# Kernel optimization log

Measured on AMD Instinct MI355X. Metric: run time of the kernel, lower is better.

## Reference

```python
import jax, jax.numpy as jnp
import numpy as np

B, T, I, E, K, J = 4, 4096, 1024, 16, 512, 1024

def setup_inputs() -> dict:
    key = jax.random.key(0)
    k1, k2, k3 = jax.random.split(key, 3)
    X = jax.random.normal(k1, (B, T, I), dtype=jnp.float32)
    ind = jax.random.randint(k2, (B, E, K), 0, T, dtype=jnp.int64)
    W = jax.random.normal(k3, (E, I, J), dtype=jnp.float32)
    return {"X": X, "ind": ind, "W": W}

def reference(X, ind, W):
    b, t, i = X.shape
    # offset each batch's indices into the flattened [B*T, I] token table
    offset = jnp.arange(b, dtype=ind.dtype)[:, None, None] * t  # [B,1,1]
    X_flat = X.reshape(b * t, i)
    X_gathered = X_flat[ind + offset]  # [B,E,K,I] irregular gather
    Y = jnp.einsum('beki,eij->bekj', X_gathered, W)  # grouped GEMM per expert
    return Y
```

## Files before the change

kernel.cpp:

```cpp
#include <hip/hip_runtime.h>

#define DI __device__ __forceinline__

constexpr int Bc = 4, Tc = 4096, Ic = 1024, Ec = 16, Kc = 512, Jc = 1024;

typedef __attribute__((ext_vector_type(8))) short short8;
typedef __attribute__((ext_vector_type(4))) float floatx4;

DI unsigned pack2_bf16(float a, float b) {
  union { float f; unsigned u; } ua, ub;
  ua.f = a; ub.f = b;
  const unsigned x = ua.u + 0x8000u;
  const unsigned y = ub.u + 0x8000u;
#if __has_builtin(__builtin_amdgcn_perm)
  return __builtin_amdgcn_perm(y, x, 0x07060302u);
#else
  return (x >> 16) | (y & 0xFFFF0000u);
#endif
}

DI void async_load16(const void* g, void* lds) {
  __builtin_amdgcn_global_load_lds((const __attribute__((address_space(1))) void*)g,
                                   (__attribute__((address_space(3))) void*)lds,
                                   16, 0, 0);
}

__global__ __launch_bounds__(256) void transpose_w(const float* __restrict__ W,
                                                   unsigned short* __restrict__ Wt) {
  __shared__ float tile[64][65];
  const int bid = blockIdx.x;
  const int jt = bid & 15;
  const int it = (bid >> 4) & 15;
  const int e  = bid >> 8;
  const int t  = threadIdx.x;

  const float* Wp = W + ((size_t)e * Ic + (size_t)it * 64) * Jc + jt * 64;
  const int jl  = (t & 15) * 4;
  const int il0 = t >> 4;
#pragma unroll
  for (int p = 0; p < 4; ++p) {
    const int il = p * 16 + il0;
    const float4 v = *(const float4*)(Wp + (size_t)il * Jc + jl);
    tile[il][jl + 0] = v.x; tile[il][jl + 1] = v.y;
    tile[il][jl + 2] = v.z; tile[il][jl + 3] = v.w;
  }
  __syncthreads();
  unsigned short* Wo = Wt + ((size_t)e * Jc + (size_t)jt * 64) * Ic + it * 64;
  const int ilw = (t & 15) * 4;
  const int jl0 = t >> 4;
#pragma unroll
  for (int p = 0; p < 4; ++p) {
    const int jlw = p * 16 + jl0;
    uint2 u;
    u.x = pack2_bf16(tile[ilw + 0][jlw], tile[ilw + 1][jlw]);
    u.y = pack2_bf16(tile[ilw + 2][jlw], tile[ilw + 3][jlw]);
    *(uint2*)(Wo + (size_t)jlw * Ic + ilw) = u;
  }
}

__global__ __launch_bounds__(256) void moe_gemm(const float* __restrict__ X,
                                                const int* __restrict__ ind,
                                                const unsigned short* __restrict__ Wt,
                                                float* __restrict__ Y) {
  __shared__ unsigned short As[128 * 32];
  __shared__ unsigned short Bs[128 * 32];
  __shared__ unsigned long long rowA[128];

  const int bid = blockIdx.x;
  const int jt = bid & 7;
  const int kt = (bid >> 3) & 3;
  const int e  = (bid >> 5) & 15;
  const int b  = bid >> 9;

  const int t = threadIdx.x;
  const int w = t >> 6;
  const int l = t & 63;

  if (t < 128) {
    const int r = ind[((b * Ec + e) * Kc) + kt * 128 + t];
    rowA[t] = (unsigned long long)(const void*)X +
              ((unsigned long long)(b * Tc + r) * (unsigned long long)Ic) * 4ull;
  }
  __syncthreads();

  const int c4 = (t & 7) * 4;
  unsigned long long abase[4];
#pragma unroll
  for (int p = 0; p < 4; ++p)
    abase[p] = rowA[p * 32 + (t >> 3)] + (unsigned long long)(c4 * 4);
  unsigned short* awr = &As[(t >> 3) * 32 + c4];

  const unsigned short* bsrc0 =
      Wt + ((size_t)(e * Jc + jt * 128 + (w * 2 + 0) * 16 + (l >> 2))) * Ic + (l & 3) * 8;
  const unsigned short* bsrc1 =
      Wt + ((size_t)(e * Jc + jt * 128 + (w * 2 + 1) * 16 + (l >> 2))) * Ic + (l & 3) * 8;
  unsigned short* bdst0 = &Bs[(w * 2 + 0) * 16 * 32];
  unsigned short* bdst1 = &Bs[(w * 2 + 1) * 16 * 32];

  floatx4 acc[4][4];
#pragma unroll
  for (int tm = 0; tm < 4; ++tm)
#pragma unroll
    for (int tn = 0; tn < 4; ++tn) acc[tm][tn] = (floatx4){0.f, 0.f, 0.f, 0.f};

  const int wm = (w & 1) * 64;
  const int wn = (w >> 1) * 64;
  const int lrow = l & 15;
  const int quad = l >> 4;

  for (int kk = 0; kk < Ic / 32; ++kk) {
    float4 av[4];
#pragma unroll
    for (int p = 0; p < 4; ++p)
      av[p] = *reinterpret_cast<const float4*>(abase[p] + (unsigned long long)(kk * 128));

    __syncthreads();

    async_load16(bsrc0 + kk * 32, bdst0);
    async_load16(bsrc1 + kk * 32, bdst1);

#pragma unroll
    for (int p = 0; p < 4; ++p) {
      uint2 u;
      u.x = pack2_bf16(av[p].x, av[p].y);
      u.y = pack2_bf16(av[p].z, av[p].w);
      *(uint2*)(awr + p * 1024) = u;
    }
    __syncthreads();

    short8 af[4], bf[4];
#pragma unroll
    for (int tm = 0; tm < 4; ++tm)
      af[tm] = *(const short8*)&As[(wm + tm * 16 + lrow) * 32 + quad * 8];
#pragma unroll
    for (int tn = 0; tn < 4; ++tn)
      bf[tn] = *(const short8*)&Bs[(wn + tn * 16 + lrow) * 32 + quad * 8];
#pragma unroll
    for (int tm = 0; tm < 4; ++tm)
#pragma unroll
      for (int tn = 0; tn < 4; ++tn)
        acc[tm][tn] = __builtin_amdgcn_mfma_f32_16x16x32_bf16(af[tm], bf[tn], acc[tm][tn], 0, 0, 0);
  }

  float* Yp = Y + ((size_t)(b * Ec + e) * Kc + (size_t)kt * 128) * Jc + jt * 128;
#pragma unroll
  for (int tm = 0; tm < 4; ++tm) {
#pragma unroll
    for (int tn = 0; tn < 4; ++tn) {
#pragma unroll
      for (int r = 0; r < 4; ++r) {
        const int row = wm + tm * 16 + quad * 4 + r;
        const int col = wn + tn * 16 + lrow;
        Yp[(size_t)row * Jc + col] = acc[tm][tn][r];
      }
    }
  }
}

extern "C" void kernel_launch(void* const* d_in, const int* in_sizes, int n_in,
                              void* d_out, int out_size, void* d_ws, size_t ws_size,
                              hipStream_t stream) {
  const float* X = (const float*)d_in[0];
  const int* ind = (const int*)d_in[1];
  const float* W = (const float*)d_in[2];
  float* Y = (float*)d_out;
  unsigned short* Wt = (unsigned short*)d_ws;

  hipLaunchKernelGGL(transpose_w, dim3(Ec * 16 * 16), dim3(256), 0, stream, W, Wt);
  hipLaunchKernelGGL(moe_gemm, dim3(Bc * Ec * 4 * 8), dim3(256), 0, stream, X, ind, Wt, Y);
}
```

Before: 356.7 us.

## Pre-gather X to bf16 buffer, pre-tile W, async-load both with swizzle

Adds a separate gather_cast kernel that gathers the indexed X rows and converts them to bf16 in a contiguous workspace. W is transposed into per-tile contiguous 128x32 blocks, so the GEMM can bring in both A and B through direct global-to-LDS async loads instead of register loads and conversion. LDS chunks are XOR-swizzled to reduce bank conflicts. The cost is an extra kernel launch and an extra write and read of the gathered X (each row is reused across 8 j-tiles, so the conversion is no longer repeated), and the GEMM main loop is still single-buffered.

```diff
diff --git a/kernel.cpp b/kernel.cpp
--- a/kernel.cpp
+++ b/kernel.cpp
@@ -25,46 +25,58 @@
                                    16, 0, 0);
 }
 
+__global__ __launch_bounds__(256) void gather_cast(const float* __restrict__ X,
+                                                   const int* __restrict__ ind,
+                                                   unsigned short* __restrict__ Xg) {
+  const int row = blockIdx.x;
+  const int t = threadIdx.x;
+  const int b = row >> 13;
+  const int r = ind[row];
+  const float4 v = *(const float4*)(X + ((size_t)(b * Tc + r)) * Ic + t * 4);
+  uint2 u;
+  u.x = pack2_bf16(v.x, v.y);
+  u.y = pack2_bf16(v.z, v.w);
+  *(uint2*)(Xg + (size_t)row * Ic + t * 4) = u;
+}
+
 __global__ __launch_bounds__(256) void transpose_w(const float* __restrict__ W,
                                                    unsigned short* __restrict__ Wt) {
-  __shared__ float tile[64][65];
+  __shared__ float tile[32][129];
   const int bid = blockIdx.x;
-  const int jt = bid & 15;
-  const int it = (bid >> 4) & 15;
+  const int kk = bid & 31;
+  const int jt = (bid >> 5) & 7;
   const int e  = bid >> 8;
   const int t  = threadIdx.x;
 
-  const float* Wp = W + ((size_t)e * Ic + (size_t)it * 64) * Jc + jt * 64;
-  const int jl  = (t & 15) * 4;
-  const int il0 = t >> 4;
+  const float* Wp = W + ((size_t)(e * Ic + kk * 32)) * Jc + jt * 128;
 #pragma unroll
   for (int p = 0; p < 4; ++p) {
-    const int il = p * 16 + il0;
-    const float4 v = *(const float4*)(Wp + (size_t)il * Jc + jl);
-    tile[il][jl + 0] = v.x; tile[il][jl + 1] = v.y;
-    tile[il][jl + 2] = v.z; tile[il][jl + 3] = v.w;
+    const int il = p * 8 + (t >> 5);
+    const int c4 = (t & 31) * 4;
+    const float4 v = *(const float4*)(Wp + (size_t)il * Jc + c4);
+    tile[il][c4 + 0] = v.x; tile[il][c4 + 1] = v.y;
+    tile[il][c4 + 2] = v.z; tile[il][c4 + 3] = v.w;
   }
   __syncthreads();
-  unsigned short* Wo = Wt + ((size_t)e * Jc + (size_t)jt * 64) * Ic + it * 64;
-  const int ilw = (t & 15) * 4;
-  const int jl0 = t >> 4;
+
+  unsigned short* out = Wt + ((size_t)((e * 8 + jt) * 32 + kk)) * 4096;
 #pragma unroll
-  for (int p = 0; p < 4; ++p) {
-    const int jlw = p * 16 + jl0;
-    uint2 u;
-    u.x = pack2_bf16(tile[ilw + 0][jlw], tile[ilw + 1][jlw]);
-    u.y = pack2_bf16(tile[ilw + 2][jlw], tile[ilw + 3][jlw]);
-    *(uint2*)(Wo + (size_t)jlw * Ic + ilw) = u;
+  for (int h = 0; h < 2; ++h) {
+    const int n   = h * 64 + (t >> 2);
+    const int il0 = (t & 3) * 8;
+    unsigned u[4];
+#pragma unroll
+    for (int q = 0; q < 4; ++q)
+      u[q] = pack2_bf16(tile[il0 + 2 * q][n], tile[il0 + 2 * q + 1][n]);
+    *(uint4*)(out + (size_t)(h * 256 + t) * 8) = *(uint4*)u;
   }
 }
 
-__global__ __launch_bounds__(256) void moe_gemm(const float* __restrict__ X,
-                                                const int* __restrict__ ind,
+__global__ __launch_bounds__(256) void moe_gemm(const unsigned short* __restrict__ Xg,
                                                 const unsigned short* __restrict__ Wt,
                                                 float* __restrict__ Y) {
   __shared__ unsigned short As[128 * 32];
   __shared__ unsigned short Bs[128 * 32];
-  __shared__ unsigned long long rowA[128];
 
   const int bid = blockIdx.x;
   const int jt = bid & 7;
@@ -75,27 +87,22 @@
   const int t = threadIdx.x;
   const int w = t >> 6;
   const int l = t & 63;
+  const int nl  = l >> 2;
+  const int csw = (l & 3) ^ (nl & 3);
 
-  if (t < 128) {
-    const int r = ind[((b * Ec + e) * Kc) + kt * 128 + t];
-    rowA[t] = (unsigned long long)(const void*)X +
-              ((unsigned long long)(b * Tc + r) * (unsigned long long)Ic) * 4ull;
+  const int R0 = (b * Ec + e) * Kc + kt * 128;
+  const unsigned short* asrc[2];
+  const unsigned short* bsrc[2];
+  unsigned short* adst[2];
+  unsigned short* bdst[2];
+#pragma unroll
+  for (int p = 0; p < 2; ++p) {
+    const int rg = w * 2 + p;
+    asrc[p] = Xg + (size_t)(R0 + rg * 16 + nl) * Ic + csw * 8;
+    bsrc[p] = Wt + ((size_t)((e * 8 + jt) * 32)) * 4096 + rg * 512 + nl * 32 + csw * 8;
+    adst[p] = &As[rg * 512];
+    bdst[p] = &Bs[rg * 512];
   }
-  __syncthreads();
-
-  const int c4 = (t & 7) * 4;
-  unsigned long long abase[4];
-#pragma unroll
-  for (int p = 0; p < 4; ++p)
-    abase[p] = rowA[p * 32 + (t >> 3)] + (unsigned long long)(c4 * 4);
-  unsigned short* awr = &As[(t >> 3) * 32 + c4];
-
-  const unsigned short* bsrc0 =
-      Wt + ((size_t)(e * Jc + jt * 128 + (w * 2 + 0) * 16 + (l >> 2))) * Ic + (l & 3) * 8;
-  const unsigned short* bsrc1 =
-      Wt + ((size_t)(e * Jc + jt * 128 + (w * 2 + 1) * 16 + (l >> 2))) * Ic + (l & 3) * 8;
-  unsigned short* bdst0 = &Bs[(w * 2 + 0) * 16 * 32];
-  unsigned short* bdst1 = &Bs[(w * 2 + 1) * 16 * 32];
 
   floatx4 acc[4][4];
 #pragma unroll
@@ -107,34 +114,24 @@
   const int wn = (w >> 1) * 64;
   const int lrow = l & 15;
   const int quad = l >> 4;
+  const int swz  = lrow & 3;
 
   for (int kk = 0; kk < Ic / 32; ++kk) {
-    float4 av[4];
+    __syncthreads();
 #pragma unroll
-    for (int p = 0; p < 4; ++p)
-      av[p] = *reinterpret_cast<const float4*>(abase[p] + (unsigned long long)(kk * 128));
-
-    __syncthreads();
-
-    async_load16(bsrc0 + kk * 32, bdst0);
-    async_load16(bsrc1 + kk * 32, bdst1);
-
-#pragma unroll
-    for (int p = 0; p < 4; ++p) {
-      uint2 u;
-      u.x = pack2_bf16(av[p].x, av[p].y);
-      u.y = pack2_bf16(av[p].z, av[p].w);
-      *(uint2*)(awr + p * 1024) = u;
+    for (int p = 0; p < 2; ++p) {
+      async_load16(asrc[p] + kk * 32, adst[p]);
+      async_load16(bsrc[p] + (size_t)kk * 4096, bdst[p]);
     }
     __syncthreads();
 
     short8 af[4], bf[4];
 #pragma unroll
     for (int tm = 0; tm < 4; ++tm)
-      af[tm] = *(const short8*)&As[(wm + tm * 16 + lrow) * 32 + quad * 8];
+      af[tm] = *(const short8*)&As[(wm + tm * 16 + lrow) * 32 + (quad ^ swz) * 8];
 #pragma unroll
     for (int tn = 0; tn < 4; ++tn)
-      bf[tn] = *(const short8*)&Bs[(wn + tn * 16 + lrow) * 32 + quad * 8];
+      bf[tn] = *(const short8*)&Bs[(wn + tn * 16 + lrow) * 32 + (quad ^ swz) * 8];
 #pragma unroll
     for (int tm = 0; tm < 4; ++tm)
 #pragma unroll
@@ -164,8 +161,11 @@
   const int* ind = (const int*)d_in[1];
   const float* W = (const float*)d_in[2];
   float* Y = (float*)d_out;
-  unsigned short* Wt = (unsigned short*)d_ws;
 
-  hipLaunchKernelGGL(transpose_w, dim3(Ec * 16 * 16), dim3(256), 0, stream, W, Wt);
-  hipLaunchKernelGGL(moe_gemm, dim3(Bc * Ec * 4 * 8), dim3(256), 0, stream, X, ind, Wt, Y);
+  unsigned short* Xg = (unsigned short*)d_ws;
+  unsigned short* Wt = (unsigned short*)d_ws + (size_t)Bc * Ec * Kc * Ic;
+
+  hipLaunchKernelGGL(gather_cast, dim3(Bc * Ec * Kc), dim3(256), 0, stream, X, ind, Xg);
+  hipLaunchKernelGGL(transpose_w, dim3(Ec * 8 * 32), dim3(256), 0, stream, W, Wt);
+  hipLaunchKernelGGL(moe_gemm, dim3(Bc * Ec * 4 * 8), dim3(256), 0, stream, Xg, Wt, Y);
 }
```

After: 355.7 us. No clear change (-0.3%).
